# Optimization experiments

Hardware: AMD Instinct MI355X
Metric: run time of the kernel (lower is better)

Reference implementation:

```python
import jax, jax.numpy as jnp
import numpy as np

N, E, F_IN, EC = 3072, 98304, 128, 3
H1, D1 = 4, 8
EC2 = H1 * EC  # 12 = edge_attr_dim2 = edge_attr_dim3
H2, D2 = 1, 8
C1, C2 = 16, 1  # DIFFPool cluster counts
NEG = 0.2


def _add_self_loops(edge_index, edge_attr, n):
    loops = jnp.arange(n, dtype=edge_index.dtype)
    ei = jnp.concatenate([edge_index, jnp.stack([loops, loops])], axis=1)
    ea = jnp.concatenate([edge_attr, jnp.ones((n, edge_attr.shape[1]), edge_attr.dtype)], axis=0)
    return ei, ea


def _egat(x, edge_index, edge_attr, w, a, heads, out_ch, n):
    # GAT-style per-destination softmax attention, modulated per edge-attr channel.
    h = (x @ w).reshape(n, heads, out_ch)                      # [N,H,D]
    row, col = edge_index[0], edge_index[1]
    alpha = jnp.einsum('ehd,hd->eh', jnp.concatenate([h[row], h[col]], axis=-1), a)
    alpha = jax.nn.leaky_relu(alpha, NEG)
    amax = jax.lax.stop_gradient(jax.ops.segment_max(alpha, row, num_segments=n))
    ex = jnp.exp(alpha - amax[row])
    denom = jax.ops.segment_sum(ex, row, num_segments=n)
    alpha = ex / (denom[row] + 1e-16)                          # [E,H]
    att = alpha[:, :, None] * edge_attr[:, None, :]            # [E,H,C]
    msg = att[:, :, :, None] * h[col][:, :, None, :]           # [E,H,C,D]
    out = jax.ops.segment_sum(msg, row, num_segments=n).reshape(n, -1)  # [N, H*C*D]
    return out, att.reshape(att.shape[0], -1)                  # e_new: [E, H*C]


def _diffpool(x, adj, S):
    s = jax.nn.softmax(S, axis=-1)                             # [Nin, Nout]
    x_new = s.T @ x
    adj_new = jnp.einsum('cim,mj->cij', jnp.einsum('ni,cnm->cim', s, adj), s)
    link = jnp.sqrt(jnp.sum((adj - (s @ s.T)[None]) ** 2)) / adj.size
    ent = -jnp.mean(jnp.sum(s * jnp.log(s + 1e-15), axis=-1))
    return x_new, adj_new, link + ent


def setup_inputs():
    key = jax.random.key(0)
    ks = jax.random.split(key, 20)
    row = jax.random.randint(ks[0], (E,), 0, N, dtype=jnp.int32)
    col = (row + jax.random.randint(ks[1], (E,), 1, N, dtype=jnp.int32)) % N  # no self loops
    g = lambda k, sh: jax.random.normal(k, sh, jnp.float32) * 0.1
    return {
        'x': jax.random.normal(ks[2], (N, F_IN), jnp.float32),
        'edge_index': jnp.stack([row, col]),
        'edge_attr': jax.random.uniform(ks[3], (E, EC), dtype=jnp.float32),
        'adj': jax.random.uniform(ks[4], (EC2, N, N), dtype=jnp.float32),
        'w1': g(ks[5], (F_IN, H1 * D1)), 'a1': g(ks[6], (H1, 2 * D1)),
        'w2': g(ks[7], (H1 * D1 * EC, H2 * D2)), 'a2': g(ks[8], (H2, 2 * D2)),
        's1': g(ks[9], (N, C1)), 's2': g(ks[10], (C1, C2)),
        'fc1_w': g(ks[11], (H2 * D2 * EC2, 128)), 'fc1_b': jnp.zeros((128,), jnp.float32),
        'fc2_w': g(ks[12], (128, 32)), 'fc2_b': jnp.zeros((32,), jnp.float32),
        'fc3_w': g(ks[13], (32, 16)), 'fc3_b': jnp.zeros((16,), jnp.float32),
        'fc4_w': g(ks[14], (16, 2)), 'fc4_b': jnp.zeros((2,), jnp.float32),
    }


def reference(x, edge_index, edge_attr, adj, w1, a1, w2, a2, s1, s2,
              fc1_w, fc1_b, fc2_w, fc2_b, fc3_w, fc3_b, fc4_w, fc4_b):
    ei, ea = _add_self_loops(edge_index, edge_attr, N)
    h, e = _egat(x, ei, ea, w1, a1, H1, D1, N)
    h = jax.nn.elu(h)
    h, e = _egat(h, ei, e, w2, a2, H2, D2, N)
    h = jax.nn.elu(h)
    h, adj1, reg1 = _diffpool(h, adj, s1)
    h, adj2, reg2 = _diffpool(h, adj1, s2)
    h = h.reshape(1, -1)                                       # [1, 8*EC2]
    h = jax.nn.elu(h @ fc1_w + fc1_b)
    h = jax.nn.elu(h @ fc2_w + fc2_b)
    h = jax.nn.elu(h @ fc3_w + fc3_b)
    h = h @ fc4_w + fc4_b
    return jax.nn.log_softmax(h, axis=1), reg1, reg2
```

## Files before the change

### kernel.cpp

```cpp
#include <hip/hip_runtime.h>
#include <hip/hip_bf16.h>

#define Nn 3072
#define E_IN 98304
#define EP (E_IN + Nn)
#define CAP 128
#define NNsq ((size_t)Nn * (size_t)Nn)

__device__ __forceinline__ float eluf(float a) { return a > 0.f ? a : (expf(a) - 1.f); }

__global__ __launch_bounds__(256) void k_softmax(const float* __restrict__ s1,
                                                 float* __restrict__ s_soft,
                                                 float* __restrict__ scal) {
    int n = blockIdx.x * 256 + threadIdx.x;
    float v[16], mx = -1e30f;
#pragma unroll
    for (int i = 0; i < 16; i++) { v[i] = s1[n * 16 + i]; mx = fmaxf(mx, v[i]); }
    float s = 0.f;
#pragma unroll
    for (int i = 0; i < 16; i++) { v[i] = expf(v[i] - mx); s += v[i]; }
    float inv = 1.f / s, ent = 0.f;
#pragma unroll
    for (int i = 0; i < 16; i++) {
        float p = v[i] * inv;
        s_soft[n * 16 + i] = p;
        ent += p * logf(p + 1e-15f);
    }
    __shared__ float wsum[4];
    for (int off = 32; off; off >>= 1) ent += __shfl_xor(ent, off);
    if ((threadIdx.x & 63) == 0) wsum[threadIdx.x >> 6] = ent;
    __syncthreads();
    if (threadIdx.x == 0) atomicAdd(&scal[2], wsum[0] + wsum[1] + wsum[2] + wsum[3]);
}

__global__ void k_bucket(const int* __restrict__ ei, int* __restrict__ counts,
                         int* __restrict__ bucket) {
    int e = blockIdx.x * 256 + threadIdx.x;
    if (e >= EP) return;
    int r = (e < E_IN) ? ei[e] : (e - E_IN);
    int pos = atomicAdd(&counts[r], 1);
    if (pos < CAP) bucket[r * CAP + pos] = e;
}

__global__ __launch_bounds__(256) void k_gemm1(const float* __restrict__ x,
                                               const float* __restrict__ w1,
                                               float* __restrict__ h1) {
    __shared__ float xs[8 * 128];
    int n0 = blockIdx.x * 8;
    for (int idx = threadIdx.x; idx < 1024; idx += 256) xs[idx] = x[(size_t)n0 * 128 + idx];
    __syncthreads();
    int r = threadIdx.x >> 5, j = threadIdx.x & 31;
    float acc = 0.f;
#pragma unroll 8
    for (int k = 0; k < 128; k++) acc += xs[r * 128 + k] * w1[k * 32 + j];
    h1[(n0 + r) * 32 + j] = acc;
}

__global__ __launch_bounds__(256) void k_egat1(const int* __restrict__ ei,
                                               const float* __restrict__ ea,
                                               const float* __restrict__ a1,
                                               const float* __restrict__ h1,
                                               const int* __restrict__ counts,
                                               const int* __restrict__ bucket,
                                               float* __restrict__ e1,
                                               float* __restrict__ hL1) {
    __shared__ float a1s[64];
    __shared__ float alphaL[4][CAP][4];
    __shared__ float eaL[4][CAP][3];
    __shared__ int   colL[4][CAP];
    int tid = threadIdx.x, w = tid >> 6, lane = tid & 63;
    if (tid < 64) a1s[tid] = a1[tid];
    __syncthreads();
    int n = blockIdx.x * 4 + w;
    int deg = counts[n]; if (deg > CAP) deg = CAP;
    const int* ei1 = ei + E_IN;
    float src[4];
#pragma unroll
    for (int h = 0; h < 4; h++) {
        float s = 0.f;
#pragma unroll
        for (int d = 0; d < 8; d++) s += h1[n * 32 + h * 8 + d] * a1s[h * 16 + d];
        src[h] = s;
    }
    float exs[4] = {0.f, 0.f, 0.f, 0.f};
    for (int sl = lane; sl < deg; sl += 64) {
        int e = bucket[n * CAP + sl];
        int col = (e < E_IN) ? ei1[e] : n;
        colL[w][sl] = col;
        float hc[32];
#pragma unroll
        for (int d = 0; d < 32; d++) hc[d] = h1[col * 32 + d];
#pragma unroll
        for (int h = 0; h < 4; h++) {
            float t = src[h];
#pragma unroll
            for (int d = 0; d < 8; d++) t += hc[h * 8 + d] * a1s[h * 16 + 8 + d];
            t = t > 0.f ? t : 0.2f * t;
            float ex = expf(t);
            alphaL[w][sl][h] = ex;
            exs[h] += ex;
        }
#pragma unroll
        for (int c = 0; c < 3; c++)
            eaL[w][sl][c] = (e < E_IN) ? ea[(size_t)e * 3 + c] : 1.0f;
    }
#pragma unroll
    for (int h = 0; h < 4; h++) {
        float v = exs[h];
        for (int off = 32; off; off >>= 1) v += __shfl_xor(v, off);
        exs[h] = v + 1e-16f;
    }
    for (int sl = lane; sl < deg; sl += 64) {
        int e = bucket[n * CAP + sl];
        float al[4];
#pragma unroll
        for (int h = 0; h < 4; h++) { al[h] = alphaL[w][sl][h] / exs[h]; alphaL[w][sl][h] = al[h]; }
#pragma unroll
        for (int h = 0; h < 4; h++)
#pragma unroll
            for (int c = 0; c < 3; c++)
                e1[(size_t)e * 12 + h * 3 + c] = al[h] * eaL[w][sl][c];
    }
    __syncthreads();
    for (int o = lane; o < 96; o += 64) {
        int h = o / 24, rem = o % 24, c = rem >> 3, d = rem & 7;
        float acc = 0.f;
        for (int sl = 0; sl < deg; sl++)
            acc += alphaL[w][sl][h] * eaL[w][sl][c] * h1[colL[w][sl] * 32 + h * 8 + d];
        hL1[(size_t)n * 96 + o] = eluf(acc);
    }
}

__global__ __launch_bounds__(256) void k_gemm2(const float* __restrict__ hL1,
                                               const float* __restrict__ w2,
                                               float* __restrict__ h2) {
    int id = blockIdx.x * 256 + threadIdx.x;
    int n = id >> 3, j = id & 7;
    float acc = 0.f;
#pragma unroll 8
    for (int k = 0; k < 96; k++) acc += hL1[(size_t)n * 96 + k] * w2[k * 8 + j];
    h2[n * 8 + j] = acc;
}

__global__ __launch_bounds__(256) void k_egat2(const int* __restrict__ ei,
                                               const float* __restrict__ e1,
                                               const float* __restrict__ a2,
                                               const float* __restrict__ h2,
                                               const int* __restrict__ counts,
                                               const int* __restrict__ bucket,
                                               float* __restrict__ hL2) {
    __shared__ float a2s[16];
    __shared__ float alphaL[4][CAP];
    __shared__ float eL[4][CAP][12];
    __shared__ int   colL[4][CAP];
    int tid = threadIdx.x, w = tid >> 6, lane = tid & 63;
    if (tid < 16) a2s[tid] = a2[tid];
    __syncthreads();
    int n = blockIdx.x * 4 + w;
    int deg = counts[n]; if (deg > CAP) deg = CAP;
    const int* ei1 = ei + E_IN;
    float src = 0.f;
#pragma unroll
    for (int d = 0; d < 8; d++) src += h2[n * 8 + d] * a2s[d];
    float exs = 0.f;
    for (int sl = lane; sl < deg; sl += 64) {
        int e = bucket[n * CAP + sl];
        int col = (e < E_IN) ? ei1[e] : n;
        colL[w][sl] = col;
        float t = src;
#pragma unroll
        for (int d = 0; d < 8; d++) t += h2[col * 8 + d] * a2s[8 + d];
        t = t > 0.f ? t : 0.2f * t;
        float ex = expf(t);
        alphaL[w][sl] = ex; exs += ex;
#pragma unroll
        for (int c = 0; c < 12; c++) eL[w][sl][c] = e1[(size_t)e * 12 + c];
    }
    for (int off = 32; off; off >>= 1) exs += __shfl_xor(exs, off);
    exs += 1e-16f;
    for (int sl = lane; sl < deg; sl += 64) alphaL[w][sl] /= exs;
    __syncthreads();
    for (int o = lane; o < 96; o += 64) {
        int c = o >> 3, d = o & 7;
        float acc = 0.f;
        for (int sl = 0; sl < deg; sl++)
            acc += alphaL[w][sl] * eL[w][sl][c] * h2[colL[w][sl] * 8 + d];
        hL2[(size_t)n * 96 + o] = eluf(acc);
    }
}

__global__ __launch_bounds__(256) void k_adj(const float* __restrict__ adj,
                                             const float* __restrict__ s_soft,
                                             float* __restrict__ tmat,
                                             float* __restrict__ scal) {
    __shared__ float snL[64 * 16];
    __shared__ float wsum[4];
    int tid = threadIdx.x;
    int m = blockIdx.x * 256 + tid;
    int c0 = blockIdx.y * 2, c1 = c0 + 1;
    int n0 = blockIdx.z * 384;
    float sm[16];
#pragma unroll
    for (int i = 0; i < 16; i++) sm[i] = s_soft[m * 16 + i];
    float t0[16], t1[16];
#pragma unroll
    for (int i = 0; i < 16; i++) { t0[i] = 0.f; t1[i] = 0.f; }
    float lsum = 0.f;
    const float* A0 = adj + (size_t)c0 * NNsq;
    const float* A1 = adj + (size_t)c1 * NNsq;
    for (int sub = 0; sub < 6; sub++) {
        int nb = n0 + sub * 64;
        __syncthreads();
        for (int l = tid; l < 1024; l += 256) snL[l] = s_soft[(size_t)nb * 16 + l];
        __syncthreads();
        for (int nn = 0; nn < 64; nn++) {
            size_t rowbase = (size_t)(nb + nn) * Nn + m;
            float a0 = A0[rowbase];
            float a1 = A1[rowbase];
            float P = 0.f;
            const float* sn = &snL[nn * 16];
#pragma unroll
            for (int i = 0; i < 16; i++) P += sn[i] * sm[i];
            float d0 = a0 - P, d1 = a1 - P;
            lsum += d0 * d0 + d1 * d1;
#pragma unroll
            for (int i = 0; i < 16; i++) { t0[i] += sn[i] * a0; t1[i] += sn[i] * a1; }
        }
    }
#pragma unroll
    for (int i = 0; i < 16; i++) {
        atomicAdd(&tmat[((size_t)c0 * 16 + i) * 3072 + m], t0[i]);
        atomicAdd(&tmat[((size_t)c1 * 16 + i) * 3072 + m], t1[i]);
    }
    for (int off = 32; off; off >>= 1) lsum += __shfl_xor(lsum, off);
    if ((tid & 63) == 0) wsum[tid >> 6] = lsum;
    __syncthreads();
    if (tid == 0) atomicAdd(&scal[0], wsum[0] + wsum[1] + wsum[2] + wsum[3]);
}

__global__ __launch_bounds__(256) void k_adj2(const float* __restrict__ tmat,
                                              const float* __restrict__ s_soft,
                                              float* __restrict__ scal) {
    int b = blockIdx.x;
    int tid = threadIdx.x;
    const float* trow = tmat + (size_t)b * 3072;
    float acc[16];
#pragma unroll
    for (int j = 0; j < 16; j++) acc[j] = 0.f;
    for (int m = tid; m < 3072; m += 256) {
        float tv = trow[m];
#pragma unroll
        for (int j = 0; j < 16; j++) acc[j] += tv * s_soft[m * 16 + j];
    }
    __shared__ float wpart[16][4];
#pragma unroll
    for (int j = 0; j < 16; j++) {
        float v = acc[j];
        for (int off = 32; off; off >>= 1) v += __shfl_xor(v, off);
        if ((tid & 63) == 0) wpart[j][tid >> 6] = v;
    }
    __syncthreads();
    if (tid < 16) {
        float v = wpart[tid][0] + wpart[tid][1] + wpart[tid][2] + wpart[tid][3];
        float d = v - 1.0f;
        atomicAdd(&scal[1], d * d);
    }
}

__global__ __launch_bounds__(256) void k_colsum(const float* __restrict__ hL2,
                                                float* __restrict__ xfin) {
    int f = blockIdx.x;
    int tid = threadIdx.x;
    float s = 0.f;
    for (int n = tid; n < 3072; n += 256) s += hL2[(size_t)n * 96 + f];
    __shared__ float wsum[4];
    for (int off = 32; off; off >>= 1) s += __shfl_xor(s, off);
    if ((tid & 63) == 0) wsum[tid >> 6] = s;
    __syncthreads();
    if (tid == 0) xfin[f] = wsum[0] + wsum[1] + wsum[2] + wsum[3];
}

__global__ void k_fc(const float* __restrict__ xfin,
                     const float* __restrict__ w1, const float* __restrict__ b1,
                     const float* __restrict__ w2, const float* __restrict__ b2,
                     const float* __restrict__ w3, const float* __restrict__ b3,
                     const float* __restrict__ w4, const float* __restrict__ b4,
                     const float* __restrict__ scal, float* __restrict__ out) {
    __shared__ float xf[96], z1[128], z2[32], z3[16], z4[2];
    int t = threadIdx.x;
    if (t < 96) xf[t] = xfin[t];
    __syncthreads();
    {
        float a = b1[t];
        for (int k = 0; k < 96; k++) a += xf[k] * w1[k * 128 + t];
        z1[t] = eluf(a);
    }
    __syncthreads();
    if (t < 32) {
        float a = b2[t];
        for (int k = 0; k < 128; k++) a += z1[k] * w2[k * 32 + t];
        z2[t] = eluf(a);
    }
    __syncthreads();
    if (t < 16) {
        float a = b3[t];
        for (int k = 0; k < 32; k++) a += z2[k] * w3[k * 16 + t];
        z3[t] = eluf(a);
    }
    __syncthreads();
    if (t < 2) {
        float a = b4[t];
        for (int k = 0; k < 16; k++) a += z3[k] * w4[k * 2 + t];
        z4[t] = a;
    }
    __syncthreads();
    if (t == 0) {
        float mx = fmaxf(z4[0], z4[1]);
        float lse = mx + logf(expf(z4[0] - mx) + expf(z4[1] - mx));
        out[0] = z4[0] - lse;
        out[1] = z4[1] - lse;
        float ent1 = -scal[2] / 3072.0f;
        float link1 = sqrtf(scal[0]) / 113246208.0f;
        out[2] = link1 + ent1;
        float link2 = sqrtf(scal[1]) / 3072.0f;
        out[3] = link2;
    }
}

extern "C" void kernel_launch(void* const* d_in, const int* in_sizes, int n_in,
                              void* d_out, int out_size, void* d_ws, size_t ws_size,
                              hipStream_t stream) {
    const float* x    = (const float*)d_in[0];
    const int*   ei   = (const int*)d_in[1];
    const float* ea   = (const float*)d_in[2];
    const float* adj  = (const float*)d_in[3];
    const float* w1   = (const float*)d_in[4];
    const float* a1   = (const float*)d_in[5];
    const float* w2   = (const float*)d_in[6];
    const float* a2   = (const float*)d_in[7];
    const float* s1   = (const float*)d_in[8];
    const float* fc1w = (const float*)d_in[10];
    const float* fc1b = (const float*)d_in[11];
    const float* fc2w = (const float*)d_in[12];
    const float* fc2b = (const float*)d_in[13];
    const float* fc3w = (const float*)d_in[14];
    const float* fc3b = (const float*)d_in[15];
    const float* fc4w = (const float*)d_in[16];
    const float* fc4b = (const float*)d_in[17];
    float* out = (float*)d_out;

    float* ws     = (float*)d_ws;
    float* tmat   = ws;
    float* xfin   = tmat + 589824;
    float* scal   = xfin + 96;
    int*   counts = (int*)(scal + 4);
    int*   bucket = counts + 3072;
    float* s_soft = (float*)(bucket + 3072 * CAP);
    float* h1     = s_soft + 3072 * 16;
    float* hL1    = h1 + 3072 * 32;
    float* h2     = hL1 + 3072 * 96;
    float* hL2    = h2 + 3072 * 8;
    float* e1     = hL2 + 3072 * 96;

    hipMemsetAsync(tmat, 0, (589824 + 96 + 4) * sizeof(float) + 3072 * sizeof(int), stream);

    k_softmax<<<12, 256, 0, stream>>>(s1, s_soft, scal);
    k_bucket<<<(EP + 255) / 256, 256, 0, stream>>>(ei, counts, bucket);
    k_gemm1<<<384, 256, 0, stream>>>(x, w1, h1);
    k_egat1<<<768, 256, 0, stream>>>(ei, ea, a1, h1, counts, bucket, e1, hL1);
    k_gemm2<<<96, 256, 0, stream>>>(hL1, w2, h2);
    k_egat2<<<768, 256, 0, stream>>>(ei, e1, a2, h2, counts, bucket, hL2);
    k_adj<<<dim3(12, 6, 8), 256, 0, stream>>>(adj, s_soft, tmat, scal);
    k_adj2<<<192, 256, 0, stream>>>(tmat, s_soft, scal);
    k_colsum<<<96, 256, 0, stream>>>(hL2, xfin);
    k_fc<<<1, 128, 0, stream>>>(xfin, fc1w, fc1b, fc2w, fc2b, fc3w, fc3b, fc4w, fc4b, scal, out);
}
```

Baseline: 870.9 us.

## Replace bucketed EGAT with edge-parallel atomics and expand link loss algebraically

Drops the per-node bucket build and recasts both EGAT layers as edge-parallel kernels. Softmax denominators and message aggregation are accumulated with global atomics, and the ELU is applied lazily in the consumers. The adjacency pass now computes the link loss as sum(adj^2) - 2*tr(s^T adj s) + 12*||s^T s||^2 through a new Gram kernel and a trace term from k_adj2, so it no longer forms s s^T inside the adj stream. It also retiles k_adj to read float4 rows. The trade-off is heavy atomic contention on hL1/hL2, and the link loss can lose precision through cancellation.

```diff
diff --git a/kernel.cpp b/kernel.cpp
--- a/kernel.cpp
+++ b/kernel.cpp
@@ -4,7 +4,6 @@
 #define Nn 3072
 #define E_IN 98304
 #define EP (E_IN + Nn)
-#define CAP 128
 #define NNsq ((size_t)Nn * (size_t)Nn)
 
 __device__ __forceinline__ float eluf(float a) { return a > 0.f ? a : (expf(a) - 1.f); }
@@ -31,15 +30,6 @@
     if ((threadIdx.x & 63) == 0) wsum[threadIdx.x >> 6] = ent;
     __syncthreads();
     if (threadIdx.x == 0) atomicAdd(&scal[2], wsum[0] + wsum[1] + wsum[2] + wsum[3]);
-}
-
-__global__ void k_bucket(const int* __restrict__ ei, int* __restrict__ counts,
-                         int* __restrict__ bucket) {
-    int e = blockIdx.x * 256 + threadIdx.x;
-    if (e >= EP) return;
-    int r = (e < E_IN) ? ei[e] : (e - E_IN);
-    int pos = atomicAdd(&counts[r], 1);
-    if (pos < CAP) bucket[r * CAP + pos] = e;
 }
 
 __global__ __launch_bounds__(256) void k_gemm1(const float* __restrict__ x,
@@ -56,186 +46,196 @@
     h1[(n0 + r) * 32 + j] = acc;
 }
 
-__global__ __launch_bounds__(256) void k_egat1(const int* __restrict__ ei,
-                                               const float* __restrict__ ea,
-                                               const float* __restrict__ a1,
-                                               const float* __restrict__ h1,
-                                               const int* __restrict__ counts,
-                                               const int* __restrict__ bucket,
-                                               float* __restrict__ e1,
-                                               float* __restrict__ hL1) {
+__global__ __launch_bounds__(256) void k_e1a(const int* __restrict__ ei,
+                                             const float* __restrict__ a1,
+                                             const float* __restrict__ h1,
+                                             float* __restrict__ ex1,
+                                             float* __restrict__ denom1) {
     __shared__ float a1s[64];
-    __shared__ float alphaL[4][CAP][4];
-    __shared__ float eaL[4][CAP][3];
-    __shared__ int   colL[4][CAP];
-    int tid = threadIdx.x, w = tid >> 6, lane = tid & 63;
-    if (tid < 64) a1s[tid] = a1[tid];
-    __syncthreads();
-    int n = blockIdx.x * 4 + w;
-    int deg = counts[n]; if (deg > CAP) deg = CAP;
-    const int* ei1 = ei + E_IN;
-    float src[4];
+    if (threadIdx.x < 64) a1s[threadIdx.x] = a1[threadIdx.x];
+    __syncthreads();
+    int e = blockIdx.x * 256 + threadIdx.x;
+    if (e >= EP) return;
+    int row = (e < E_IN) ? ei[e] : (e - E_IN);
+    int col = (e < E_IN) ? ei[E_IN + e] : (e - E_IN);
+    const float4* H = (const float4*)h1;
+    float hr[32], hc[32];
+#pragma unroll
+    for (int k = 0; k < 8; k++) {
+        float4 r4 = H[row * 8 + k], c4 = H[col * 8 + k];
+        hr[k*4+0]=r4.x; hr[k*4+1]=r4.y; hr[k*4+2]=r4.z; hr[k*4+3]=r4.w;
+        hc[k*4+0]=c4.x; hc[k*4+1]=c4.y; hc[k*4+2]=c4.z; hc[k*4+3]=c4.w;
+    }
 #pragma unroll
     for (int h = 0; h < 4; h++) {
-        float s = 0.f;
-#pragma unroll
-        for (int d = 0; d < 8; d++) s += h1[n * 32 + h * 8 + d] * a1s[h * 16 + d];
-        src[h] = s;
-    }
-    float exs[4] = {0.f, 0.f, 0.f, 0.f};
-    for (int sl = lane; sl < deg; sl += 64) {
-        int e = bucket[n * CAP + sl];
-        int col = (e < E_IN) ? ei1[e] : n;
-        colL[w][sl] = col;
-        float hc[32];
-#pragma unroll
-        for (int d = 0; d < 32; d++) hc[d] = h1[col * 32 + d];
-#pragma unroll
-        for (int h = 0; h < 4; h++) {
-            float t = src[h];
-#pragma unroll
-            for (int d = 0; d < 8; d++) t += hc[h * 8 + d] * a1s[h * 16 + 8 + d];
-            t = t > 0.f ? t : 0.2f * t;
-            float ex = expf(t);
-            alphaL[w][sl][h] = ex;
-            exs[h] += ex;
-        }
-#pragma unroll
-        for (int c = 0; c < 3; c++)
-            eaL[w][sl][c] = (e < E_IN) ? ea[(size_t)e * 3 + c] : 1.0f;
-    }
-#pragma unroll
-    for (int h = 0; h < 4; h++) {
-        float v = exs[h];
-        for (int off = 32; off; off >>= 1) v += __shfl_xor(v, off);
-        exs[h] = v + 1e-16f;
-    }
-    for (int sl = lane; sl < deg; sl += 64) {
-        int e = bucket[n * CAP + sl];
-        float al[4];
-#pragma unroll
-        for (int h = 0; h < 4; h++) { al[h] = alphaL[w][sl][h] / exs[h]; alphaL[w][sl][h] = al[h]; }
-#pragma unroll
-        for (int h = 0; h < 4; h++)
-#pragma unroll
-            for (int c = 0; c < 3; c++)
-                e1[(size_t)e * 12 + h * 3 + c] = al[h] * eaL[w][sl][c];
-    }
-    __syncthreads();
-    for (int o = lane; o < 96; o += 64) {
-        int h = o / 24, rem = o % 24, c = rem >> 3, d = rem & 7;
-        float acc = 0.f;
-        for (int sl = 0; sl < deg; sl++)
-            acc += alphaL[w][sl][h] * eaL[w][sl][c] * h1[colL[w][sl] * 32 + h * 8 + d];
-        hL1[(size_t)n * 96 + o] = eluf(acc);
-    }
-}
-
-__global__ __launch_bounds__(256) void k_gemm2(const float* __restrict__ hL1,
+        float t = 0.f;
+#pragma unroll
+        for (int d = 0; d < 8; d++)
+            t += hr[h*8+d] * a1s[h*16+d] + hc[h*8+d] * a1s[h*16+8+d];
+        t = t > 0.f ? t : 0.2f * t;
+        float ex = expf(t);
+        ex1[e * 4 + h] = ex;
+        atomicAdd(&denom1[row * 4 + h], ex);
+    }
+}
+
+__global__ __launch_bounds__(256) void k_e1b(const int* __restrict__ ei,
+                                             const float* __restrict__ ea,
+                                             const float* __restrict__ h1,
+                                             const float* __restrict__ ex1,
+                                             const float* __restrict__ denom1,
+                                             float* __restrict__ e1,
+                                             float* __restrict__ hL1acc) {
+    int id = blockIdx.x * 256 + threadIdx.x;
+    if (id >= 4 * EP) return;
+    int e = id >> 2, h = id & 3;
+    int row = (e < E_IN) ? ei[e] : (e - E_IN);
+    int col = (e < E_IN) ? ei[E_IN + e] : (e - E_IN);
+    float alpha = ex1[e * 4 + h] / (denom1[row * 4 + h] + 1e-16f);
+    float eac[3];
+#pragma unroll
+    for (int c = 0; c < 3; c++) eac[c] = (e < E_IN) ? ea[(size_t)e * 3 + c] : 1.0f;
+    const float4* H = (const float4*)h1;
+    float4 q0 = H[col * 8 + h * 2], q1 = H[col * 8 + h * 2 + 1];
+    float hcv[8] = {q0.x,q0.y,q0.z,q0.w,q1.x,q1.y,q1.z,q1.w};
+#pragma unroll
+    for (int c = 0; c < 3; c++) {
+        float ac = alpha * eac[c];
+        e1[(size_t)e * 12 + h * 3 + c] = ac;
+        float* dst = &hL1acc[(size_t)row * 96 + h * 24 + c * 8];
+#pragma unroll
+        for (int d = 0; d < 8; d++) atomicAdd(dst + d, ac * hcv[d]);
+    }
+}
+
+__global__ __launch_bounds__(256) void k_gemm2(const float* __restrict__ hL1acc,
                                                const float* __restrict__ w2,
                                                float* __restrict__ h2) {
     int id = blockIdx.x * 256 + threadIdx.x;
     int n = id >> 3, j = id & 7;
     float acc = 0.f;
 #pragma unroll 8
-    for (int k = 0; k < 96; k++) acc += hL1[(size_t)n * 96 + k] * w2[k * 8 + j];
+    for (int k = 0; k < 96; k++) acc += eluf(hL1acc[(size_t)n * 96 + k]) * w2[k * 8 + j];
     h2[n * 8 + j] = acc;
 }
 
-__global__ __launch_bounds__(256) void k_egat2(const int* __restrict__ ei,
-                                               const float* __restrict__ e1,
-                                               const float* __restrict__ a2,
-                                               const float* __restrict__ h2,
-                                               const int* __restrict__ counts,
-                                               const int* __restrict__ bucket,
-                                               float* __restrict__ hL2) {
+__global__ __launch_bounds__(256) void k_e2a(const int* __restrict__ ei,
+                                             const float* __restrict__ a2,
+                                             const float* __restrict__ h2,
+                                             float* __restrict__ ex2,
+                                             float* __restrict__ denom2) {
     __shared__ float a2s[16];
-    __shared__ float alphaL[4][CAP];
-    __shared__ float eL[4][CAP][12];
-    __shared__ int   colL[4][CAP];
-    int tid = threadIdx.x, w = tid >> 6, lane = tid & 63;
-    if (tid < 16) a2s[tid] = a2[tid];
-    __syncthreads();
-    int n = blockIdx.x * 4 + w;
-    int deg = counts[n]; if (deg > CAP) deg = CAP;
-    const int* ei1 = ei + E_IN;
-    float src = 0.f;
-#pragma unroll
-    for (int d = 0; d < 8; d++) src += h2[n * 8 + d] * a2s[d];
-    float exs = 0.f;
-    for (int sl = lane; sl < deg; sl += 64) {
-        int e = bucket[n * CAP + sl];
-        int col = (e < E_IN) ? ei1[e] : n;
-        colL[w][sl] = col;
-        float t = src;
-#pragma unroll
-        for (int d = 0; d < 8; d++) t += h2[col * 8 + d] * a2s[8 + d];
-        t = t > 0.f ? t : 0.2f * t;
-        float ex = expf(t);
-        alphaL[w][sl] = ex; exs += ex;
-#pragma unroll
-        for (int c = 0; c < 12; c++) eL[w][sl][c] = e1[(size_t)e * 12 + c];
-    }
-    for (int off = 32; off; off >>= 1) exs += __shfl_xor(exs, off);
-    exs += 1e-16f;
-    for (int sl = lane; sl < deg; sl += 64) alphaL[w][sl] /= exs;
-    __syncthreads();
-    for (int o = lane; o < 96; o += 64) {
-        int c = o >> 3, d = o & 7;
-        float acc = 0.f;
-        for (int sl = 0; sl < deg; sl++)
-            acc += alphaL[w][sl] * eL[w][sl][c] * h2[colL[w][sl] * 8 + d];
-        hL2[(size_t)n * 96 + o] = eluf(acc);
-    }
+    if (threadIdx.x < 16) a2s[threadIdx.x] = a2[threadIdx.x];
+    __syncthreads();
+    int e = blockIdx.x * 256 + threadIdx.x;
+    if (e >= EP) return;
+    int row = (e < E_IN) ? ei[e] : (e - E_IN);
+    int col = (e < E_IN) ? ei[E_IN + e] : (e - E_IN);
+    const float4* H = (const float4*)h2;
+    float4 r0 = H[row * 2], r1 = H[row * 2 + 1];
+    float4 c0 = H[col * 2], c1 = H[col * 2 + 1];
+    float t = r0.x*a2s[0]+r0.y*a2s[1]+r0.z*a2s[2]+r0.w*a2s[3]
+            + r1.x*a2s[4]+r1.y*a2s[5]+r1.z*a2s[6]+r1.w*a2s[7]
+            + c0.x*a2s[8]+c0.y*a2s[9]+c0.z*a2s[10]+c0.w*a2s[11]
+            + c1.x*a2s[12]+c1.y*a2s[13]+c1.z*a2s[14]+c1.w*a2s[15];
+    t = t > 0.f ? t : 0.2f * t;
+    float ex = expf(t);
+    ex2[e] = ex;
+    atomicAdd(&denom2[row], ex);
+}
+
+__global__ __launch_bounds__(256) void k_e2b(const int* __restrict__ ei,
+                                             const float* __restrict__ e1,
+                                             const float* __restrict__ h2,
+                                             const float* __restrict__ ex2,
+                                             const float* __restrict__ denom2,
+                                             float* __restrict__ hL2acc) {
+    int id = blockIdx.x * 256 + threadIdx.x;
+    if (id >= 12 * EP) return;
+    int e = id / 12, c = id % 12;
+    int row = (e < E_IN) ? ei[e] : (e - E_IN);
+    int col = (e < E_IN) ? ei[E_IN + e] : (e - E_IN);
+    float w = (ex2[e] / (denom2[row] + 1e-16f)) * e1[(size_t)e * 12 + c];
+    const float4* H = (const float4*)h2;
+    float4 c0 = H[col * 2], c1 = H[col * 2 + 1];
+    float hcv[8] = {c0.x,c0.y,c0.z,c0.w,c1.x,c1.y,c1.z,c1.w};
+    float* dst = &hL2acc[(size_t)row * 96 + c * 8];
+#pragma unroll
+    for (int d = 0; d < 8; d++) atomicAdd(dst + d, w * hcv[d]);
 }
 
 __global__ __launch_bounds__(256) void k_adj(const float* __restrict__ adj,
                                              const float* __restrict__ s_soft,
                                              float* __restrict__ tmat,
                                              float* __restrict__ scal) {
-    __shared__ float snL[64 * 16];
+    __shared__ float4 snL[128 * 4];
     __shared__ float wsum[4];
     int tid = threadIdx.x;
-    int m = blockIdx.x * 256 + tid;
-    int c0 = blockIdx.y * 2, c1 = c0 + 1;
-    int n0 = blockIdx.z * 384;
-    float sm[16];
-#pragma unroll
-    for (int i = 0; i < 16; i++) sm[i] = s_soft[m * 16 + i];
-    float t0[16], t1[16];
-#pragma unroll
-    for (int i = 0; i < 16; i++) { t0[i] = 0.f; t1[i] = 0.f; }
-    float lsum = 0.f;
-    const float* A0 = adj + (size_t)c0 * NNsq;
-    const float* A1 = adj + (size_t)c1 * NNsq;
-    for (int sub = 0; sub < 6; sub++) {
-        int nb = n0 + sub * 64;
-        __syncthreads();
-        for (int l = tid; l < 1024; l += 256) snL[l] = s_soft[(size_t)nb * 16 + l];
-        __syncthreads();
-        for (int nn = 0; nn < 64; nn++) {
-            size_t rowbase = (size_t)(nb + nn) * Nn + m;
-            float a0 = A0[rowbase];
-            float a1 = A1[rowbase];
-            float P = 0.f;
-            const float* sn = &snL[nn * 16];
-#pragma unroll
-            for (int i = 0; i < 16; i++) P += sn[i] * sm[i];
-            float d0 = a0 - P, d1 = a1 - P;
-            lsum += d0 * d0 + d1 * d1;
-#pragma unroll
-            for (int i = 0; i < 16; i++) { t0[i] += sn[i] * a0; t1[i] += sn[i] * a1; }
+    int c  = blockIdx.y;
+    int nb = blockIdx.z * 128;
+    int m  = blockIdx.x * 1024 + tid * 4;
+    const float4* S4 = (const float4*)s_soft;
+    for (int l = tid; l < 512; l += 256) snL[l] = S4[(size_t)nb * 4 + l];
+    __syncthreads();
+    float4 t[16];
+#pragma unroll
+    for (int i = 0; i < 16; i++) t[i] = make_float4(0.f, 0.f, 0.f, 0.f);
+    float sq = 0.f;
+    const float* A = adj + (size_t)c * NNsq + (size_t)nb * Nn + m;
+#pragma unroll 2
+    for (int nn = 0; nn < 128; nn++) {
+        float4 a = *(const float4*)(A + (size_t)nn * Nn);
+        sq = fmaf(a.x, a.x, sq); sq = fmaf(a.y, a.y, sq);
+        sq = fmaf(a.z, a.z, sq); sq = fmaf(a.w, a.w, sq);
+#pragma unroll
+        for (int k = 0; k < 4; k++) {
+            float4 s4 = snL[nn * 4 + k];
+            t[k*4+0].x = fmaf(s4.x, a.x, t[k*4+0].x); t[k*4+0].y = fmaf(s4.x, a.y, t[k*4+0].y);
+            t[k*4+0].z = fmaf(s4.x, a.z, t[k*4+0].z); t[k*4+0].w = fmaf(s4.x, a.w, t[k*4+0].w);
+            t[k*4+1].x = fmaf(s4.y, a.x, t[k*4+1].x); t[k*4+1].y = fmaf(s4.y, a.y, t[k*4+1].y);
+            t[k*4+1].z = fmaf(s4.y, a.z, t[k*4+1].z); t[k*4+1].w = fmaf(s4.y, a.w, t[k*4+1].w);
+            t[k*4+2].x = fmaf(s4.z, a.x, t[k*4+2].x); t[k*4+2].y = fmaf(s4.z, a.y, t[k*4+2].y);
+            t[k*4+2].z = fmaf(s4.z, a.z, t[k*4+2].z); t[k*4+2].w = fmaf(s4.z, a.w, t[k*4+2].w);
+            t[k*4+3].x = fmaf(s4.w, a.x, t[k*4+3].x); t[k*4+3].y = fmaf(s4.w, a.y, t[k*4+3].y);
+            t[k*4+3].z = fmaf(s4.w, a.z, t[k*4+3].z); t[k*4+3].w = fmaf(s4.w, a.w, t[k*4+3].w);
         }
     }
 #pragma unroll
     for (int i = 0; i < 16; i++) {
-        atomicAdd(&tmat[((size_t)c0 * 16 + i) * 3072 + m], t0[i]);
-        atomicAdd(&tmat[((size_t)c1 * 16 + i) * 3072 + m], t1[i]);
-    }
-    for (int off = 32; off; off >>= 1) lsum += __shfl_xor(lsum, off);
-    if ((tid & 63) == 0) wsum[tid >> 6] = lsum;
+        float* dst = &tmat[((size_t)c * 16 + i) * 3072 + m];
+        atomicAdd(dst + 0, t[i].x); atomicAdd(dst + 1, t[i].y);
+        atomicAdd(dst + 2, t[i].z); atomicAdd(dst + 3, t[i].w);
+    }
+    for (int off = 32; off; off >>= 1) sq += __shfl_xor(sq, off);
+    if ((tid & 63) == 0) wsum[tid >> 6] = sq;
     __syncthreads();
     if (tid == 0) atomicAdd(&scal[0], wsum[0] + wsum[1] + wsum[2] + wsum[3]);
+}
+
+__global__ __launch_bounds__(256) void k_gram(const float* __restrict__ s_soft,
+                                              float* __restrict__ scal) {
+    int i = blockIdx.x;
+    int tid = threadIdx.x;
+    float acc[16];
+#pragma unroll
+    for (int j = 0; j < 16; j++) acc[j] = 0.f;
+    for (int n = tid; n < 3072; n += 256) {
+        float si = s_soft[n * 16 + i];
+#pragma unroll
+        for (int j = 0; j < 16; j++) acc[j] += si * s_soft[n * 16 + j];
+    }
+    __shared__ float wpart[16][4];
+#pragma unroll
+    for (int j = 0; j < 16; j++) {
+        float v = acc[j];
+        for (int off = 32; off; off >>= 1) v += __shfl_xor(v, off);
+        if ((tid & 63) == 0) wpart[j][tid >> 6] = v;
+    }
+    __syncthreads();
+    if (tid < 16) {
+        float g = wpart[tid][0] + wpart[tid][1] + wpart[tid][2] + wpart[tid][3];
+        atomicAdd(&scal[3], 12.0f * g * g);
+    }
 }
 
 __global__ __launch_bounds__(256) void k_adj2(const float* __restrict__ tmat,
@@ -264,15 +264,16 @@
         float v = wpart[tid][0] + wpart[tid][1] + wpart[tid][2] + wpart[tid][3];
         float d = v - 1.0f;
         atomicAdd(&scal[1], d * d);
-    }
-}
-
-__global__ __launch_bounds__(256) void k_colsum(const float* __restrict__ hL2,
+        if (tid == (b & 15)) atomicAdd(&scal[4], v);
+    }
+}
+
+__global__ __launch_bounds__(256) void k_colsum(const float* __restrict__ hL2acc,
                                                 float* __restrict__ xfin) {
     int f = blockIdx.x;
     int tid = threadIdx.x;
     float s = 0.f;
-    for (int n = tid; n < 3072; n += 256) s += hL2[(size_t)n * 96 + f];
+    for (int n = tid; n < 3072; n += 256) s += eluf(hL2acc[(size_t)n * 96 + f]);
     __shared__ float wsum[4];
     for (int off = 32; off; off >>= 1) s += __shfl_xor(s, off);
     if ((tid & 63) == 0) wsum[tid >> 6] = s;
@@ -320,7 +321,8 @@
         out[0] = z4[0] - lse;
         out[1] = z4[1] - lse;
         float ent1 = -scal[2] / 3072.0f;
-        float link1 = sqrtf(scal[0]) / 113246208.0f;
+        float l1sq = scal[0] - 2.0f * scal[4] + scal[3];
+        float link1 = sqrtf(fmaxf(l1sq, 0.f)) / 113246208.0f;
         out[2] = link1 + ent1;
         float link2 = sqrtf(scal[1]) / 3072.0f;
         out[3] = link2;
@@ -349,29 +351,34 @@
     const float* fc4b = (const float*)d_in[17];
     float* out = (float*)d_out;
 
-    float* ws     = (float*)d_ws;
-    float* tmat   = ws;
-    float* xfin   = tmat + 589824;
-    float* scal   = xfin + 96;
-    int*   counts = (int*)(scal + 4);
-    int*   bucket = counts + 3072;
-    float* s_soft = (float*)(bucket + 3072 * CAP);
-    float* h1     = s_soft + 3072 * 16;
-    float* hL1    = h1 + 3072 * 32;
-    float* h2     = hL1 + 3072 * 96;
-    float* hL2    = h2 + 3072 * 8;
-    float* e1     = hL2 + 3072 * 96;
-
-    hipMemsetAsync(tmat, 0, (589824 + 96 + 4) * sizeof(float) + 3072 * sizeof(int), stream);
+    float* ws      = (float*)d_ws;
+    float* tmat    = ws;
+    float* hL1acc  = tmat + 589824;
+    float* hL2acc  = hL1acc + 294912;
+    float* denom1  = hL2acc + 294912;
+    float* denom2  = denom1 + 12288;
+    float* xfin    = denom2 + 3072;
+    float* scal    = xfin + 96;
+    const size_t ZN = 589824 + 294912 + 294912 + 12288 + 3072 + 96 + 8;
+    float* s_soft  = scal + 8;
+    float* h1      = s_soft + 49152;
+    float* h2      = h1 + 98304;
+    float* ex1     = h2 + 24576;
+    float* ex2     = ex1 + 405504;
+    float* e1      = ex2 + 101376;
+
+    hipMemsetAsync(tmat, 0, ZN * sizeof(float), stream);
 
     k_softmax<<<12, 256, 0, stream>>>(s1, s_soft, scal);
-    k_bucket<<<(EP + 255) / 256, 256, 0, stream>>>(ei, counts, bucket);
     k_gemm1<<<384, 256, 0, stream>>>(x, w1, h1);
-    k_egat1<<<768, 256, 0, stream>>>(ei, ea, a1, h1, counts, bucket, e1, hL1);
-    k_gemm2<<<96, 256, 0, stream>>>(hL1, w2, h2);
-    k_egat2<<<768, 256, 0, stream>>>(ei, e1, a2, h2, counts, bucket, hL2);
-    k_adj<<<dim3(12, 6, 8), 256, 0, stream>>>(adj, s_soft, tmat, scal);
+    k_e1a<<<(EP + 255) / 256, 256, 0, stream>>>(ei, a1, h1, ex1, denom1);
+    k_e1b<<<(4 * EP + 255) / 256, 256, 0, stream>>>(ei, ea, h1, ex1, denom1, e1, hL1acc);
+    k_gemm2<<<96, 256, 0, stream>>>(hL1acc, w2, h2);
+    k_e2a<<<(EP + 255) / 256, 256, 0, stream>>>(ei, a2, h2, ex2, denom2);
+    k_e2b<<<(12 * EP + 255) / 256, 256, 0, stream>>>(ei, e1, h2, ex2, denom2, hL2acc);
+    k_adj<<<dim3(3, 12, 24), 256, 0, stream>>>(adj, s_soft, tmat, scal);
+    k_gram<<<16, 256, 0, stream>>>(s_soft, scal);
     k_adj2<<<192, 256, 0, stream>>>(tmat, s_soft, scal);
-    k_colsum<<<96, 256, 0, stream>>>(hL2, xfin);
+    k_colsum<<<96, 256, 0, stream>>>(hL2acc, xfin);
     k_fc<<<1, 128, 0, stream>>>(xfin, fc1w, fc1b, fc2w, fc2b, fc3w, fc3b, fc4w, fc4b, scal, out);
 }
```

Result: slower. 1.684 ms (+93.4%).
